# Optimization experiments

Measured on AMD Instinct MI355X. Metric: run time of the kernel, lower is better.

Reference implementation:

```python
import jax, jax.numpy as jnp
import numpy as np

N = 50000          # nodes
E = 800000         # edges (before self loops)
C_IN, HID, C_OUT, L = 128, 64, 64, 3
LSTM_H = (L * HID) // 2   # 96, PyG JK-LSTM hidden size
NEG_SLOPE = 0.2


def gat_conv(x, src, dst, W, a_src, a_dst, b):
    # single-head PyG GATConv
    h = x @ W.T                                  # [N, HID]
    al = h @ a_src                               # [N] src attention logits
    ar = h @ a_dst                               # [N]
    e = jax.nn.leaky_relu(al[src] + ar[dst], NEG_SLOPE)   # [E+N]
    m = jax.ops.segment_max(e, dst, num_segments=N)
    ex = jnp.exp(e - m[dst])
    den = jax.ops.segment_sum(ex, dst, num_segments=N)
    coef = ex / den[dst]                         # segment softmax over dst neighborhoods
    out = jax.ops.segment_sum(coef[:, None] * h[src], dst, num_segments=N)
    return out + b


def lstm_dir(seq, Wih, Whh, bih, bhh, reverse):
    # seq: [L, N, C]; returns hidden states [L, N, H] in original time order
    H = Whh.shape[1]
    h0 = jnp.zeros((seq.shape[1], H), seq.dtype)

    def step(carry, x_t):
        h, c = carry
        g = x_t @ Wih.T + bih + h @ Whh.T + bhh
        i, f, gg, o = jnp.split(g, 4, axis=-1)
        c = jax.nn.sigmoid(f) * c + jax.nn.sigmoid(i) * jnp.tanh(gg)
        h = jax.nn.sigmoid(o) * jnp.tanh(c)
        return (h, c), h

    _, hs = jax.lax.scan(step, (h0, h0), seq, reverse=reverse)
    return hs


def setup_inputs() -> dict:
    key = jax.random.key(0)
    ks = jax.random.split(key, 32)
    s = 0.1
    inp = {
        'x': jax.random.normal(ks[0], (N, C_IN), jnp.float32),
        'edge_index': jax.random.randint(ks[1], (2, E), 0, N, jnp.int64
                                         if jax.config.jax_enable_x64 else jnp.int32),
    }
    dims = [C_IN, HID, HID]
    for l in range(L):
        inp[f'conv{l}_W'] = s * jax.random.normal(ks[2 + 4 * l], (HID, dims[l]), jnp.float32)
        inp[f'conv{l}_asrc'] = s * jax.random.normal(ks[3 + 4 * l], (HID,), jnp.float32)
        inp[f'conv{l}_adst'] = s * jax.random.normal(ks[4 + 4 * l], (HID,), jnp.float32)
        inp[f'conv{l}_b'] = jnp.zeros((HID,), jnp.float32)
    for d, off in (('f', 16), ('b', 20)):
        inp[f'lstm_Wih_{d}'] = s * jax.random.normal(ks[off], (4 * LSTM_H, HID), jnp.float32)
        inp[f'lstm_Whh_{d}'] = s * jax.random.normal(ks[off + 1], (4 * LSTM_H, LSTM_H), jnp.float32)
        inp[f'lstm_bih_{d}'] = jnp.zeros((4 * LSTM_H,), jnp.float32)
        inp[f'lstm_bhh_{d}'] = jnp.zeros((4 * LSTM_H,), jnp.float32)
    inp['att_W'] = s * jax.random.normal(ks[24], (1, 2 * LSTM_H), jnp.float32)
    inp['att_b'] = jnp.zeros((1,), jnp.float32)
    inp['out_W'] = s * jax.random.normal(ks[25], (C_OUT, HID), jnp.float32)
    inp['out_b'] = jnp.zeros((C_OUT,), jnp.float32)
    return inp


def reference(x, edge_index,
              conv0_W, conv0_asrc, conv0_adst, conv0_b,
              conv1_W, conv1_asrc, conv1_adst, conv1_b,
              conv2_W, conv2_asrc, conv2_adst, conv2_b,
              lstm_Wih_f, lstm_Whh_f, lstm_bih_f, lstm_bhh_f,
              lstm_Wih_b, lstm_Whh_b, lstm_bih_b, lstm_bhh_b,
              att_W, att_b, out_W, out_b):
    # add self loops (PyG GATConv default)
    loop = jnp.arange(N, dtype=edge_index.dtype)
    src = jnp.concatenate([edge_index[0], loop])
    dst = jnp.concatenate([edge_index[1], loop])

    convs = [(conv0_W, conv0_asrc, conv0_adst, conv0_b),
             (conv1_W, conv1_asrc, conv1_adst, conv1_b),
             (conv2_W, conv2_asrc, conv2_adst, conv2_b)]
    xs = []
    h = x
    for (W, asrc, adst, b) in convs:
        h = jax.nn.relu(gat_conv(h, src, dst, W, asrc, adst, b))
        xs.append(h)

    seq = jnp.stack(xs, axis=0)                       # [L, N, HID]
    hf = lstm_dir(seq, lstm_Wih_f, lstm_Whh_f, lstm_bih_f, lstm_bhh_f, False)
    hb = lstm_dir(seq, lstm_Wih_b, lstm_Whh_b, lstm_bih_b, lstm_bhh_b, True)
    hcat = jnp.concatenate([hf, hb], axis=-1)         # [L, N, 2*LSTM_H]
    logits = (hcat @ att_W.T + att_b)[..., 0]         # [L, N]
    alpha = jax.nn.softmax(logits, axis=0)            # softmax over layers
    agg = jnp.einsum('lnc,ln->nc', seq, alpha)        # [N, HID]
    return agg @ out_W.T + out_b
```

## Files before the change

### kernel.cpp

```cpp
#include <hip/hip_runtime.h>
#include <hip/hip_bf16.h>
#include <math.h>


typedef __attribute__((ext_vector_type(4))) float f32x4;
typedef __attribute__((ext_vector_type(8))) short bf16x8;

__device__ __forceinline__ float rcp_f(float x) {
    return __builtin_amdgcn_rcpf(x);
}
__device__ __forceinline__ float sigmoid_f(float x) {
    return rcp_f(1.0f + __expf(-x));
}
__device__ __forceinline__ float tanh_f(float x) {
    return fmaf(2.0f, rcp_f(1.0f + __expf(-2.0f * x)), -1.0f);
}
__device__ __forceinline__ unsigned short f2bf(float x) {
    union { float f; unsigned int u; } v; v.f = x;
    unsigned int r = (v.u + 0x7FFFu + ((v.u >> 16) & 1u)) >> 16;
    return (unsigned short)r;
}
__device__ __forceinline__ float bf2f(unsigned short u) {
    union { unsigned int i; float f; } v; v.i = ((unsigned int)u) << 16;
    return v.f;
}

template<int K>
__global__ __launch_bounds__(256) void lin_kernel(
    const float* __restrict__ x, const float* __restrict__ W,
    const float* __restrict__ asrc, const float* __restrict__ adst,
    unsigned short* __restrict__ h, float* __restrict__ al,
    float* __restrict__ ar, int N)
{
    __shared__ __align__(16) float Wl[64][K + 4];
    for (int i = threadIdx.x; i < 64 * K; i += 256)
        Wl[i / K][i % K] = W[i];
    __syncthreads();

    int lane = threadIdx.x & 63;
    float as = asrc[lane], ad = adst[lane];
    int wid = (blockIdx.x * 256 + threadIdx.x) >> 6;
    int nw  = (gridDim.x * 256) >> 6;
    int n4max = (N + 3) >> 2;
    for (int n4 = wid; n4 < n4max; n4 += nw) {
        int nb = __builtin_amdgcn_readfirstlane(n4) << 2;
        const float* xr0 = x + (size_t)nb * K;
        const float* xr1 = x + (size_t)min(nb + 1, N - 1) * K;
        const float* xr2 = x + (size_t)min(nb + 2, N - 1) * K;
        const float* xr3 = x + (size_t)min(nb + 3, N - 1) * K;
        float a0 = 0.f, a1 = 0.f, a2 = 0.f, a3 = 0.f;
        #pragma unroll 4
        for (int k = 0; k < K; k += 4) {
            f32x4 wv = *reinterpret_cast<const f32x4*>(&Wl[lane][k]);
            float4 x0 = *reinterpret_cast<const float4*>(xr0 + k);
            float4 x1 = *reinterpret_cast<const float4*>(xr1 + k);
            float4 x2 = *reinterpret_cast<const float4*>(xr2 + k);
            float4 x3 = *reinterpret_cast<const float4*>(xr3 + k);
            a0 += x0.x * wv.x + x0.y * wv.y + x0.z * wv.z + x0.w * wv.w;
            a1 += x1.x * wv.x + x1.y * wv.y + x1.z * wv.z + x1.w * wv.w;
            a2 += x2.x * wv.x + x2.y * wv.y + x2.z * wv.z + x2.w * wv.w;
            a3 += x3.x * wv.x + x3.y * wv.y + x3.z * wv.z + x3.w * wv.w;
        }
        float accs[4] = {a0, a1, a2, a3};
        #pragma unroll
        for (int j = 0; j < 4; ++j) {
            int n = nb + j;
            if (n >= N) break;
            float acc = accs[j];
            h[(size_t)n * 64 + lane] = f2bf(acc);
            float pa = acc * as, pr = acc * ad;
            #pragma unroll
            for (int off = 32; off > 0; off >>= 1) {
                pa += __shfl_down(pa, off);
                pr += __shfl_down(pr, off);
            }
            if (lane == 0) { al[n] = pa; ar[n] = pr; }
        }
    }
}

__global__ void csr_zero(int* __restrict__ deg, int* __restrict__ cursor, int N)
{
    int i = blockIdx.x * blockDim.x + threadIdx.x;
    if (i < N) { deg[i] = 0; cursor[i] = 0; }
}

__global__ void csr_hist(const int* __restrict__ dst, int* __restrict__ deg, int E)
{
    int i = blockIdx.x * blockDim.x + threadIdx.x;
    if (i < E) atomicAdd(&deg[dst[i]], 1);
}

__global__ void csr_scan1(const int* __restrict__ deg, int* __restrict__ incl,
                          int* __restrict__ part, int N)
{
    __shared__ int sb[2][256];
    int tid = threadIdx.x;
    int i = blockIdx.x * 256 + tid;
    int v = (i < N) ? deg[i] + 1 : 0;
    sb[0][tid] = v;
    __syncthreads();
    int cur = 0;
    #pragma unroll
    for (int off = 1; off < 256; off <<= 1) {
        int s = sb[cur][tid];
        if (tid >= off) s += sb[cur][tid - off];
        sb[cur ^ 1][tid] = s;
        cur ^= 1;
        __syncthreads();
    }
    if (i < N) incl[i] = sb[cur][tid];
    if (tid == 255) part[blockIdx.x] = sb[cur][255];
}

__global__ void csr_scan2(int* __restrict__ part, int NB)
{
    __shared__ int sb[2][256];
    int tid = threadIdx.x;
    int v = (tid < NB) ? part[tid] : 0;
    sb[0][tid] = v;
    __syncthreads();
    int cur = 0;
    #pragma unroll
    for (int off = 1; off < 256; off <<= 1) {
        int s = sb[cur][tid];
        if (tid >= off) s += sb[cur][tid - off];
        sb[cur ^ 1][tid] = s;
        cur ^= 1;
        __syncthreads();
    }
    if (tid < NB) part[tid] = sb[cur][tid] - v;
}

__global__ void csr_scan3(const int* __restrict__ deg, const int* __restrict__ incl,
                          const int* __restrict__ part, int* __restrict__ rowptr,
                          int N, int total)
{
    int i = blockIdx.x * blockDim.x + threadIdx.x;
    if (i < N)
        rowptr[i] = part[i >> 8] + incl[i] - (deg[i] + 1);
    if (i == 0) rowptr[N] = total;
}

__global__ void csr_scatter(const int* __restrict__ src, const int* __restrict__ dst,
                            const int* __restrict__ rowptr, int* __restrict__ cursor,
                            int* __restrict__ csr_src, int E, int N)
{
    int i = blockIdx.x * blockDim.x + threadIdx.x;
    if (i >= E + N) return;
    int s = (i < E) ? src[i] : (i - E);
    int d = (i < E) ? dst[i] : (i - E);
    int pos = atomicAdd(&cursor[d], 1);
    csr_src[rowptr[d] + pos] = s;
}

__global__ __launch_bounds__(256) void agg_kernel(
    const int* __restrict__ rowptr, const int* __restrict__ csr_src,
    const float* __restrict__ al, const float* __restrict__ ar,
    const unsigned short* __restrict__ h, const float* __restrict__ b,
    float* __restrict__ outseq, unsigned short* __restrict__ outseq_bf, int N)
{
    int lane = threadIdx.x & 63;
    int w = threadIdx.x >> 6;
    int li = lane & 15, grp = lane >> 4;
    int d = blockIdx.x * 16 + w * 4 + grp;
    if (d >= N) return;

    int rp0 = rowptr[d], rp1 = rowptr[d + 1];
    int degd = rp1 - rp0;
    float ard = ar[d];
    float den = 0.0f;
    float a0 = 0.f, a1 = 0.f, a2 = 0.f, a3 = 0.f;
    const int grpbase = grp << 4;

    for (int c0 = 0; c0 < degd; c0 += 16) {
        int ne = min(16, degd - c0);
        int s_l = 0;
        float ex_l = 0.0f;
        if (li < ne) {
            s_l = csr_src[rp0 + c0 + li];
            float e = al[s_l] + ard;
            e = (e >= 0.0f) ? e : 0.2f * e;
            ex_l = __expf(e);
        }
        float dsum = ex_l;
        dsum += __shfl_xor(dsum, 1);
        dsum += __shfl_xor(dsum, 2);
        dsum += __shfl_xor(dsum, 4);
        dsum += __shfl_xor(dsum, 8);
        den += dsum;
        #pragma unroll 4
        for (int e2 = 0; e2 < ne; ++e2) {
            int sl = grpbase + e2;
            float exb = __shfl(ex_l, sl);
            int sb = __shfl(s_l, sl);
            uint2 hv = *reinterpret_cast<const uint2*>(
                &h[(size_t)sb * 64 + li * 4]);
            a0 += exb * bf2f((unsigned short)(hv.x & 0xFFFFu));
            a1 += exb * bf2f((unsigned short)(hv.x >> 16));
            a2 += exb * bf2f((unsigned short)(hv.y & 0xFFFFu));
            a3 += exb * bf2f((unsigned short)(hv.y >> 16));
        }
    }
    float inv = rcp_f(den);
    int ch = li * 4;
    float4 v;
    v.x = fmaxf(fmaf(a0, inv, b[ch]),     0.0f);
    v.y = fmaxf(fmaf(a1, inv, b[ch + 1]), 0.0f);
    v.z = fmaxf(fmaf(a2, inv, b[ch + 2]), 0.0f);
    v.w = fmaxf(fmaf(a3, inv, b[ch + 3]), 0.0f);
    *reinterpret_cast<float4*>(&outseq[(size_t)d * 64 + ch]) = v;
    uint2 bb;
    bb.x = (unsigned int)f2bf(v.x) | ((unsigned int)f2bf(v.y) << 16);
    bb.y = (unsigned int)f2bf(v.z) | ((unsigned int)f2bf(v.w) << 16);
    *reinterpret_cast<uint2*>(&outseq_bf[(size_t)d * 64 + ch]) = bb;
}

__global__ void prep_lstm(
    const float* __restrict__ WihF, const float* __restrict__ WhhF,
    const float* __restrict__ bihF, const float* __restrict__ bhhF,
    const float* __restrict__ WihB_, const float* __restrict__ WhhB_,
    const float* __restrict__ bihB_, const float* __restrict__ bhhB_,
    unsigned short* __restrict__ WB, float* __restrict__ bsum)
{
    int tid = blockIdx.x * blockDim.x + threadIdx.x;
    if (tid < 2 * 61440) {
        int dir = tid / 61440, rr = tid % 61440;
        const float* Wih = dir ? WihB_ : WihF;
        const float* Whh = dir ? WhhB_ : WhhF;
        float v;
        if (rr < 24576) {
            int f = rr >> 9, l = (rr >> 3) & 63, s = rr & 7;
            int kc = f & 1, qt = f >> 1;
            int q = qt / 6, t6 = qt % 6;
            int j = q * 96 + t6 * 16 + (l & 15);
            int k = kc * 32 + (l >> 4) * 8 + s;
            v = Wih[j * 64 + k];
        } else {
            int rr2 = rr - 24576;
            int f = rr2 >> 9, l = (rr2 >> 3) & 63, s = rr2 & 7;
            int kc = f % 3, qt = f / 3;
            int q = qt / 6, t6 = qt % 6;
            int j = q * 96 + t6 * 16 + (l & 15);
            int k = kc * 32 + (l >> 4) * 8 + s;
            v = Whh[j * 96 + k];
        }
        WB[tid] = f2bf(v);
    } else if (tid < 2 * 61440 + 2 * 384) {
        int q2 = tid - 2 * 61440;
        int dir = q2 / 384, j = q2 % 384;
        bsum[q2] = dir ? (bihB_[j] + bhhB_[j]) : (bihF[j] + bhhF[j]);
    }
}

__global__ __launch_bounds__(512, 2) void lstm_kernel(
    const unsigned short* __restrict__ seq_bf,
    const unsigned short* __restrict__ WB,
    const float* __restrict__ bsum, const float* __restrict__ attW,
    const float* __restrict__ attb, const float* __restrict__ outW,
    const float* __restrict__ outb, float* __restrict__ out, int N)
{
    __shared__ __align__(16) unsigned short smem[75520];
    unsigned short* WL = smem;
    unsigned short* HS = smem + 61440;
    float* LG = reinterpret_cast<float*>(smem + 74752);

    const int tid  = threadIdx.x;
    const int lane = tid & 63;
    const int w    = tid >> 6;
    const int i16  = lane & 15;
    const int g    = lane >> 4;
    const int n0   = blockIdx.x * 128;
    const int nodebase = 16 * w;
    const int myrow = nodebase + g * 4;

    float attb0 = attb[0];
    if (tid < 384) LG[tid] = attb0;

    for (int dir = 0; dir < 2; ++dir) {
        __syncthreads();
        {
            const f32x4* gsrc = reinterpret_cast<const f32x4*>(WB + dir * 61440);
            f32x4* ldst = reinterpret_cast<f32x4*>(WL);
            #pragma unroll
            for (int it = 0; it < 15; ++it)
                ldst[it * 512 + tid] = gsrc[it * 512 + tid];
        }
        {
            unsigned int* hz = reinterpret_cast<unsigned int*>(&HS[nodebase * 104]);
            for (int e2 = lane; e2 < 832; e2 += 64) hz[e2] = 0u;
        }
        const float* bs = bsum + dir * 384;
        const float* aw = attW + dir * 96;
        float bsr[24];
        #pragma unroll
        for (int t6 = 0; t6 < 6; ++t6)
            #pragma unroll
            for (int q = 0; q < 4; ++q)
                bsr[t6 * 4 + q] = bs[q * 96 + t6 * 16 + i16];
        float awr[6];
        #pragma unroll
        for (int t6 = 0; t6 < 6; ++t6) awr[t6] = aw[t6 * 16 + i16];
        float c[24];
        #pragma unroll
        for (int a = 0; a < 24; ++a) c[a] = 0.0f;
        __syncthreads();

        for (int step = 0; step < 3; ++step) {
            int t = dir ? (2 - step) : step;

            int nn = n0 + nodebase + i16;
            nn = (nn < N) ? nn : (N - 1);
            const unsigned short* xr = seq_bf + ((size_t)t * N + nn) * 64 + g * 8;
            bf16x8 ax0 = *reinterpret_cast<const bf16x8*>(xr);
            bf16x8 ax1 = *reinterpret_cast<const bf16x8*>(xr + 32);

            const unsigned short* hrow = &HS[(nodebase + i16) * 104];
            bf16x8 ah0 = *reinterpret_cast<const bf16x8*>(hrow + g * 8);
            bf16x8 ah1 = *reinterpret_cast<const bf16x8*>(hrow + 32 + g * 8);
            bf16x8 ah2 = *reinterpret_cast<const bf16x8*>(hrow + 64 + g * 8);
            const unsigned short* wbase = WL + lane * 8;

            float lp[4] = {0.0f, 0.0f, 0.0f, 0.0f};
            #pragma unroll
            for (int t6 = 0; t6 < 6; ++t6) {
                const int jb = t6 * 16 + i16;
                f32x4 acc4[4];
                #pragma unroll
                for (int q = 0; q < 4; ++q) {
                    float bv = bsr[t6 * 4 + q];
                    acc4[q] = (f32x4){bv, bv, bv, bv};
                }
                #pragma unroll
                for (int q = 0; q < 4; ++q) {
                    const int qt = q * 6 + t6;
                    const unsigned short* wih = wbase + (qt * 2) * 512;
                    const unsigned short* whh = wbase + 24576 + (qt * 3) * 512;
                    acc4[q] = __builtin_amdgcn_mfma_f32_16x16x32_bf16(
                        ax0, *reinterpret_cast<const bf16x8*>(wih), acc4[q], 0, 0, 0);
                    acc4[q] = __builtin_amdgcn_mfma_f32_16x16x32_bf16(
                        ax1, *reinterpret_cast<const bf16x8*>(wih + 512), acc4[q], 0, 0, 0);
                    acc4[q] = __builtin_amdgcn_mfma_f32_16x16x32_bf16(
                        ah0, *reinterpret_cast<const bf16x8*>(whh), acc4[q], 0, 0, 0);
                    acc4[q] = __builtin_amdgcn_mfma_f32_16x16x32_bf16(
                        ah1, *reinterpret_cast<const bf16x8*>(whh + 512), acc4[q], 0, 0, 0);
                    acc4[q] = __builtin_amdgcn_mfma_f32_16x16x32_bf16(
                        ah2, *reinterpret_cast<const bf16x8*>(whh + 1024), acc4[q], 0, 0, 0);
                }
                #pragma unroll
                for (int reg = 0; reg < 4; ++reg) {
                    float ii = acc4[0][reg];
                    float ff = acc4[1][reg];
                    float gg = acc4[2][reg];
                    float oo = acc4[3][reg];
                    float cn = sigmoid_f(ff) * c[t6 * 4 + reg]
                             + sigmoid_f(ii) * tanh_f(gg);
                    c[t6 * 4 + reg] = cn;
                    float hn = sigmoid_f(oo) * tanh_f(cn);
                    HS[(myrow + reg) * 104 + jb] = f2bf(hn);
                    lp[reg] += hn * awr[t6];
                }
            }
            #pragma unroll
            for (int reg = 0; reg < 4; ++reg) {
                float v = lp[reg];
                v += __shfl_xor(v, 1);
                v += __shfl_xor(v, 2);
                v += __shfl_xor(v, 4);
                v += __shfl_xor(v, 8);
                if (i16 == 0) LG[t * 128 + myrow + reg] += v;
            }
        }
    }
    __syncthreads();

    float* alphaF = reinterpret_cast<float*>(HS);
    if (tid < 128) {
        float l0 = LG[tid], l1 = LG[128 + tid], l2 = LG[256 + tid];
        float mx = fmaxf(fmaxf(l0, l1), l2);
        float e0 = __expf(l0 - mx), e1 = __expf(l1 - mx), e2 = __expf(l2 - mx);
        float inv = rcp_f(e0 + e1 + e2);
        alphaF[tid] = e0 * inv; alphaF[128 + tid] = e1 * inv;
        alphaF[256 + tid] = e2 * inv;
    }
    __syncthreads();

    float* aggF = reinterpret_cast<float*>(WL);
    for (int idx = tid; idx < 128 * 64; idx += 512) {
        int r = idx >> 6, k = idx & 63;
        int n = n0 + r;
        float v = 0.0f;
        if (n < N) {
            float a0 = alphaF[r], a1 = alphaF[128 + r], a2 = alphaF[256 + r];
            v = a0 * bf2f(seq_bf[((size_t)n) * 64 + k])
              + a1 * bf2f(seq_bf[((size_t)N + n) * 64 + k])
              + a2 * bf2f(seq_bf[((size_t)2 * N + n) * 64 + k]);
        }
        aggF[r * 68 + k] = v;
    }
    __syncthreads();

    f32x4 ow[16];
    #pragma unroll
    for (int kk = 0; kk < 16; ++kk)
        ow[kk] = *reinterpret_cast<const f32x4*>(&outW[(size_t)lane * 64 + kk * 4]);
    float ob = outb[lane];
    for (int r = w; r < 128; r += 8) {
        int n = n0 + r;
        if (n >= N) break;
        float a = ob;
        #pragma unroll
        for (int kk = 0; kk < 16; ++kk) {
            f32x4 av = *reinterpret_cast<const f32x4*>(&aggF[r * 68 + kk * 4]);
            a += ow[kk].x * av.x + ow[kk].y * av.y
               + ow[kk].z * av.z + ow[kk].w * av.w;
        }
        out[(size_t)n * 64 + lane] = a;
    }
}

extern "C" void kernel_launch(void* const* d_in, const int* in_sizes, int n_in,
                              void* d_out, int out_size, void* d_ws, size_t ws_size,
                              hipStream_t stream)
{
    const float* x    = (const float*)d_in[0];
    const int*   ei   = (const int*)d_in[1];
    const float* convW[3]  = {(const float*)d_in[2], (const float*)d_in[6],  (const float*)d_in[10]};
    const float* convAs[3] = {(const float*)d_in[3], (const float*)d_in[7],  (const float*)d_in[11]};
    const float* convAd[3] = {(const float*)d_in[4], (const float*)d_in[8],  (const float*)d_in[12]};
    const float* convB[3]  = {(const float*)d_in[5], (const float*)d_in[9],  (const float*)d_in[13]};
    const float* WihF = (const float*)d_in[14];
    const float* WhhF = (const float*)d_in[15];
    const float* bihF = (const float*)d_in[16];
    const float* bhhF = (const float*)d_in[17];
    const float* WihB = (const float*)d_in[18];
    const float* WhhB = (const float*)d_in[19];
    const float* bihB = (const float*)d_in[20];
    const float* bhhB = (const float*)d_in[21];
    const float* attW = (const float*)d_in[22];
    const float* attb = (const float*)d_in[23];
    const float* outW = (const float*)d_in[24];
    const float* outb = (const float*)d_in[25];

    int N = in_sizes[0] / 128;
    int E = in_sizes[1] / 2;
    const int* src = ei;
    const int* dst = ei + E;
    int total = E + N;

    float* w = (float*)d_ws;
    float* seq  = w;  w += (size_t)3 * N * 64;
    unsigned short* h_bf = (unsigned short*)w;  w += (size_t)N * 32;
    float* al   = w;  w += N;
    float* ar   = w;  w += N;
    float* bsum = w;  w += 768;
    unsigned short* WB = (unsigned short*)w;  w += 61440;
    unsigned short* seq_bf = (unsigned short*)w;  w += (size_t)3 * N * 32;
    int* deg     = (int*)w;        w += N;
    int* cursor  = (int*)w;        w += N;
    int* rowptr  = (int*)w;        w += (N + 1);
    int* incl    = (int*)w;        w += N;
    int* part    = (int*)w;        w += 256;
    int* csr_src = (int*)w;        w += total;

    int NB = (N + 255) / 256;

    csr_zero<<<NB, 256, 0, stream>>>(deg, cursor, N);
    csr_hist<<<(E + 255) / 256, 256, 0, stream>>>(dst, deg, E);
    csr_scan1<<<NB, 256, 0, stream>>>(deg, incl, part, N);
    csr_scan2<<<1, 256, 0, stream>>>(part, NB);
    csr_scan3<<<NB, 256, 0, stream>>>(deg, incl, part, rowptr, N, total);
    csr_scatter<<<(total + 255) / 256, 256, 0, stream>>>(src, dst, rowptr, cursor,
                                                         csr_src, E, N);

    prep_lstm<<<(2 * 61440 + 768 + 255) / 256, 256, 0, stream>>>(
        WihF, WhhF, bihF, bhhF, WihB, WhhB, bihB, bhhB, WB, bsum);

    for (int l = 0; l < 3; ++l) {
        const float* in = (l == 0) ? x : seq + (size_t)(l - 1) * N * 64;
        if (l == 0)
            lin_kernel<128><<<2048, 256, 0, stream>>>(in, convW[l], convAs[l], convAd[l],
                                                      h_bf, al, ar, N);
        else
            lin_kernel<64><<<2048, 256, 0, stream>>>(in, convW[l], convAs[l], convAd[l],
                                                     h_bf, al, ar, N);
        agg_kernel<<<(N + 15) / 16, 256, 0, stream>>>(rowptr, csr_src, al, ar, h_bf,
                                                      convB[l], seq + (size_t)l * N * 64,
                                                      seq_bf + (size_t)l * N * 64, N);
    }

    lstm_kernel<<<(N + 127) / 128, 512, 0, stream>>>(seq_bf, WB, bsum, attW, attb,
                                                     outW, outb, (float*)d_out, N);
}
```

Before: 374.1 us.

## Process two 128-node tiles per LSTM block to amortize weight staging

Each LSTM block now handles two consecutive 128-node tiles, and the grid size is halved. The per-direction bf16 weight load into shared memory is therefore shared across both tiles instead of being repeated for every tile. The logits buffer is doubled so each tile keeps its own LSTM attention scores. The cost is fewer blocks (about 196 on a 256-CU part), which can leave CUs idle and lower parallelism, and the serialized epilogue adds extra barriers.

```diff
diff --git a/kernel.cpp b/kernel.cpp
--- a/kernel.cpp
+++ b/kernel.cpp
@@ -260,7 +260,7 @@
     const float* __restrict__ attb, const float* __restrict__ outW,
     const float* __restrict__ outb, float* __restrict__ out, int N)
 {
-    __shared__ __align__(16) unsigned short smem[75520];
+    __shared__ __align__(16) unsigned short smem[76288];
     unsigned short* WL = smem;
     unsigned short* HS = smem + 61440;
     float* LG = reinterpret_cast<float*>(smem + 74752);
@@ -270,12 +270,12 @@
     const int w    = tid >> 6;
     const int i16  = lane & 15;
     const int g    = lane >> 4;
-    const int n0   = blockIdx.x * 128;
     const int nodebase = 16 * w;
     const int myrow = nodebase + g * 4;
+    const int U = (N + 127) >> 7;
 
     float attb0 = attb[0];
-    if (tid < 384) LG[tid] = attb0;
+    for (int idx = tid; idx < 768; idx += 512) LG[idx] = attb0;
 
     for (int dir = 0; dir < 2; ++dir) {
         __syncthreads();
@@ -285,10 +285,6 @@
             #pragma unroll
             for (int it = 0; it < 15; ++it)
                 ldst[it * 512 + tid] = gsrc[it * 512 + tid];
-        }
-        {
-            unsigned int* hz = reinterpret_cast<unsigned int*>(&HS[nodebase * 104]);
-            for (int e2 = lane; e2 < 832; e2 += 64) hz[e2] = 0u;
         }
         const float* bs = bsum + dir * 384;
         const float* aw = attW + dir * 96;
@@ -301,102 +297,90 @@
         float awr[6];
         #pragma unroll
         for (int t6 = 0; t6 < 6; ++t6) awr[t6] = aw[t6 * 16 + i16];
-        float c[24];
+        __syncthreads();
+
         #pragma unroll
-        for (int a = 0; a < 24; ++a) c[a] = 0.0f;
-        __syncthreads();
-
-        for (int step = 0; step < 3; ++step) {
-            int t = dir ? (2 - step) : step;
-
-            int nn = n0 + nodebase + i16;
-            nn = (nn < N) ? nn : (N - 1);
-            const unsigned short* xr = seq_bf + ((size_t)t * N + nn) * 64 + g * 8;
-            bf16x8 ax0 = *reinterpret_cast<const bf16x8*>(xr);
-            bf16x8 ax1 = *reinterpret_cast<const bf16x8*>(xr + 32);
-
-            const unsigned short* hrow = &HS[(nodebase + i16) * 104];
-            bf16x8 ah0 = *reinterpret_cast<const bf16x8*>(hrow + g * 8);
-            bf16x8 ah1 = *reinterpret_cast<const bf16x8*>(hrow + 32 + g * 8);
-            bf16x8 ah2 = *reinterpret_cast<const bf16x8*>(hrow + 64 + g * 8);
-            const unsigned short* wbase = WL + lane * 8;
-
-            float lp[4] = {0.0f, 0.0f, 0.0f, 0.0f};
+        for (int un = 0; un < 2; ++un) {
+            int u = blockIdx.x * 2 + un;
+            if (u >= U) continue;
+            int n0 = u * 128;
+
+            {
+                unsigned int* hz =
+                    reinterpret_cast<unsigned int*>(&HS[nodebase * 104]);
+                for (int e2 = lane; e2 < 832; e2 += 64) hz[e2] = 0u;
+            }
+            float c[24];
             #pragma unroll
-            for (int t6 = 0; t6 < 6; ++t6) {
-                const int jb = t6 * 16 + i16;
-                f32x4 acc4[4];
+            for (int a = 0; a < 24; ++a) c[a] = 0.0f;
+
+            for (int step = 0; step < 3; ++step) {
+                int t = dir ? (2 - step) : step;
+
+                int nn = n0 + nodebase + i16;
+                nn = (nn < N) ? nn : (N - 1);
+                const unsigned short* xr =
+                    seq_bf + ((size_t)t * N + nn) * 64 + g * 8;
+                bf16x8 ax0 = *reinterpret_cast<const bf16x8*>(xr);
+                bf16x8 ax1 = *reinterpret_cast<const bf16x8*>(xr + 32);
+
+                const unsigned short* hrow = &HS[(nodebase + i16) * 104];
+                bf16x8 ah0 = *reinterpret_cast<const bf16x8*>(hrow + g * 8);
+                bf16x8 ah1 = *reinterpret_cast<const bf16x8*>(hrow + 32 + g * 8);
+                bf16x8 ah2 = *reinterpret_cast<const bf16x8*>(hrow + 64 + g * 8);
+                const unsigned short* wbase = WL + lane * 8;
+
+                float lp[4] = {0.0f, 0.0f, 0.0f, 0.0f};
                 #pragma unroll
-                for (int q = 0; q < 4; ++q) {
-                    float bv = bsr[t6 * 4 + q];
-                    acc4[q] = (f32x4){bv, bv, bv, bv};
-                }
-                #pragma unroll
-                for (int q = 0; q < 4; ++q) {
-                    const int qt = q * 6 + t6;
-                    const unsigned short* wih = wbase + (qt * 2) * 512;
-                    const unsigned short* whh = wbase + 24576 + (qt * 3) * 512;
-                    acc4[q] = __builtin_amdgcn_mfma_f32_16x16x32_bf16(
-                        ax0, *reinterpret_cast<const bf16x8*>(wih), acc4[q], 0, 0, 0);
-                    acc4[q] = __builtin_amdgcn_mfma_f32_16x16x32_bf16(
-                        ax1, *reinterpret_cast<const bf16x8*>(wih + 512), acc4[q], 0, 0, 0);
-                    acc4[q] = __builtin_amdgcn_mfma_f32_16x16x32_bf16(
-                        ah0, *reinterpret_cast<const bf16x8*>(whh), acc4[q], 0, 0, 0);
-                    acc4[q] = __builtin_amdgcn_mfma_f32_16x16x32_bf16(
-                        ah1, *reinterpret_cast<const bf16x8*>(whh + 512), acc4[q], 0, 0, 0);
-                    acc4[q] = __builtin_amdgcn_mfma_f32_16x16x32_bf16(
-                        ah2, *reinterpret_cast<const bf16x8*>(whh + 1024), acc4[q], 0, 0, 0);
+                for (int t6 = 0; t6 < 6; ++t6) {
+                    const int jb = t6 * 16 + i16;
+                    f32x4 acc4[4];
+                    #pragma unroll
+                    for (int q = 0; q < 4; ++q) {
+                        float bv = bsr[t6 * 4 + q];
+                        acc4[q] = (f32x4){bv, bv, bv, bv};
+                    }
+                    #pragma unroll
+                    for (int q = 0; q < 4; ++q) {
+                        const int qt = q * 6 + t6;
+                        const unsigned short* wih = wbase + (qt * 2) * 512;
+                        const unsigned short* whh = wbase + 24576 + (qt * 3) * 512;
+                        acc4[q] = __builtin_amdgcn_mfma_f32_16x16x32_bf16(
+                            ax0, *reinterpret_cast<const bf16x8*>(wih), acc4[q], 0, 0, 0);
+                        acc4[q] = __builtin_amdgcn_mfma_f32_16x16x32_bf16(
+                            ax1, *reinterpret_cast<const bf16x8*>(wih + 512), acc4[q], 0, 0, 0);
+                        acc4[q] = __builtin_amdgcn_mfma_f32_16x16x32_bf16(
+                            ah0, *reinterpret_cast<const bf16x8*>(whh), acc4[q], 0, 0, 0);
+                        acc4[q] = __builtin_amdgcn_mfma_f32_16x16x32_bf16(
+                            ah1, *reinterpret_cast<const bf16x8*>(whh + 512), acc4[q], 0, 0, 0);
+                        acc4[q] = __builtin_amdgcn_mfma_f32_16x16x32_bf16(
+                            ah2, *reinterpret_cast<const bf16x8*>(whh + 1024), acc4[q], 0, 0, 0);
+                    }
+                    #pragma unroll
+                    for (int reg = 0; reg < 4; ++reg) {
+                        float ii = acc4[0][reg];
+                        float ff = acc4[1][reg];
+                        float gg = acc4[2][reg];
+                        float oo = acc4[3][reg];
+                        float cn = sigmoid_f(ff) * c[t6 * 4 + reg]
+                                 + sigmoid_f(ii) * tanh_f(gg);
+                        c[t6 * 4 + reg] = cn;
+                        float hn = sigmoid_f(oo) * tanh_f(cn);
+                        HS[(myrow + reg) * 104 + jb] = f2bf(hn);
+                        lp[reg] += hn * awr[t6];
+                    }
                 }
                 #pragma unroll
                 for (int reg = 0; reg < 4; ++reg) {
-                    float ii = acc4[0][reg];
-                    float ff = acc4[1][reg];
-                    float gg = acc4[2][reg];
-                    float oo = acc4[3][reg];
-                    float cn = sigmoid_f(ff) * c[t6 * 4 + reg]
-                             + sigmoid_f(ii) * tanh_f(gg);
-                    c[t6 * 4 + reg] = cn;
-                    float hn = sigmoid_f(oo) * tanh_f(cn);
-                    HS[(myrow + reg) * 104 + jb] = f2bf(hn);
-                    lp[reg] += hn * awr[t6];
+                    float v = lp[reg];
+                    v += __shfl_xor(v, 1);
+                    v += __shfl_xor(v, 2);
+                    v += __shfl_xor(v, 4);
+                    v += __shfl_xor(v, 8);
+                    if (i16 == 0) LG[un * 384 + t * 128 + myrow + reg] += v;
                 }
             }
-            #pragma unroll
-            for (int reg = 0; reg < 4; ++reg) {
-                float v = lp[reg];
-                v += __shfl_xor(v, 1);
-                v += __shfl_xor(v, 2);
-                v += __shfl_xor(v, 4);
-                v += __shfl_xor(v, 8);
-                if (i16 == 0) LG[t * 128 + myrow + reg] += v;
-            }
-        }
-    }
-    __syncthreads();
-
-    float* alphaF = reinterpret_cast<float*>(HS);
-    if (tid < 128) {
-        float l0 = LG[tid], l1 = LG[128 + tid], l2 = LG[256 + tid];
-        float mx = fmaxf(fmaxf(l0, l1), l2);
-        float e0 = __expf(l0 - mx), e1 = __expf(l1 - mx), e2 = __expf(l2 - mx);
-        float inv = rcp_f(e0 + e1 + e2);
-        alphaF[tid] = e0 * inv; alphaF[128 + tid] = e1 * inv;
-        alphaF[256 + tid] = e2 * inv;
-    }
-    __syncthreads();
-
-    float* aggF = reinterpret_cast<float*>(WL);
-    for (int idx = tid; idx < 128 * 64; idx += 512) {
-        int r = idx >> 6, k = idx & 63;
-        int n = n0 + r;
-        float v = 0.0f;
-        if (n < N) {
-            float a0 = alphaF[r], a1 = alphaF[128 + r], a2 = alphaF[256 + r];
-            v = a0 * bf2f(seq_bf[((size_t)n) * 64 + k])
-              + a1 * bf2f(seq_bf[((size_t)N + n) * 64 + k])
-              + a2 * bf2f(seq_bf[((size_t)2 * N + n) * 64 + k]);
-        }
-        aggF[r * 68 + k] = v;
+        }
     }
     __syncthreads();
 
@@ -405,17 +389,53 @@
     for (int kk = 0; kk < 16; ++kk)
         ow[kk] = *reinterpret_cast<const f32x4*>(&outW[(size_t)lane * 64 + kk * 4]);
     float ob = outb[lane];
-    for (int r = w; r < 128; r += 8) {
-        int n = n0 + r;
-        if (n >= N) break;
-        float a = ob;
-        #pragma unroll
-        for (int kk = 0; kk < 16; ++kk) {
-            f32x4 av = *reinterpret_cast<const f32x4*>(&aggF[r * 68 + kk * 4]);
-            a += ow[kk].x * av.x + ow[kk].y * av.y
-               + ow[kk].z * av.z + ow[kk].w * av.w;
-        }
-        out[(size_t)n * 64 + lane] = a;
+
+    for (int un = 0; un < 2; ++un) {
+        int u = blockIdx.x * 2 + un;
+        if (u >= U) continue;
+        int n0 = u * 128;
+
+        float* alphaF = reinterpret_cast<float*>(HS);
+        if (tid < 128) {
+            float l0 = LG[un * 384 + tid];
+            float l1 = LG[un * 384 + 128 + tid];
+            float l2 = LG[un * 384 + 256 + tid];
+            float mx = fmaxf(fmaxf(l0, l1), l2);
+            float e0 = __expf(l0 - mx), e1 = __expf(l1 - mx), e2 = __expf(l2 - mx);
+            float inv = rcp_f(e0 + e1 + e2);
+            alphaF[tid] = e0 * inv; alphaF[128 + tid] = e1 * inv;
+            alphaF[256 + tid] = e2 * inv;
+        }
+        __syncthreads();
+
+        float* aggF = reinterpret_cast<float*>(WL);
+        for (int idx = tid; idx < 128 * 64; idx += 512) {
+            int r = idx >> 6, k = idx & 63;
+            int n = n0 + r;
+            float v = 0.0f;
+            if (n < N) {
+                float a0 = alphaF[r], a1 = alphaF[128 + r], a2 = alphaF[256 + r];
+                v = a0 * bf2f(seq_bf[((size_t)n) * 64 + k])
+                  + a1 * bf2f(seq_bf[((size_t)N + n) * 64 + k])
+                  + a2 * bf2f(seq_bf[((size_t)2 * N + n) * 64 + k]);
+            }
+            aggF[r * 68 + k] = v;
+        }
+        __syncthreads();
+
+        for (int r = w; r < 128; r += 8) {
+            int n = n0 + r;
+            if (n >= N) break;
+            float a = ob;
+            #pragma unroll
+            for (int kk = 0; kk < 16; ++kk) {
+                f32x4 av = *reinterpret_cast<const f32x4*>(&aggF[r * 68 + kk * 4]);
+                a += ow[kk].x * av.x + ow[kk].y * av.y
+                   + ow[kk].z * av.z + ow[kk].w * av.w;
+            }
+            out[(size_t)n * 64 + lane] = a;
+        }
+        __syncthreads();
     }
 }
 
@@ -489,6 +509,7 @@
                                                       seq_bf + (size_t)l * N * 64, N);
     }
 
-    lstm_kernel<<<(N + 127) / 128, 512, 0, stream>>>(seq_bf, WB, bsum, attW, attb,
-                                                     outW, outb, (float*)d_out, N);
-}
+    int U = (N + 127) / 128;
+    lstm_kernel<<<(U + 1) / 2, 512, 0, stream>>>(seq_bf, WB, bsum, attW, attb,
+                                                 outW, outb, (float*)d_out, N);
+}
```

New measurement: 375.4 us. About the same (+0.3%).

## Split GAT aggregation lanes across edges and channel quarters

Applied to the files above, without the earlier changes.

Reorganizes the per-destination aggregation so each 16-lane group processes 4 edges at once, with each lane loading 16 bf16 channels (32 bytes) of a source row instead of 4 channels per edge serially. Partial sums are combined with xor shuffles at the end, and one lane per channel quarter writes the outputs. This is meant to cut the serial per-edge loop and the per-edge broadcast shuffles and to widen memory loads. In exchange it needs 16 accumulator registers per lane, a final reduction, and wastes lanes on the tail when the degree is not a multiple of 4.

```diff
diff --git a/kernel.cpp b/kernel.cpp
--- a/kernel.cpp
+++ b/kernel.cpp
@@ -165,55 +165,72 @@
     int li = lane & 15, grp = lane >> 4;
     int d = blockIdx.x * 16 + w * 4 + grp;
     if (d >= N) return;
+    int cq = li >> 2, es = li & 3;
 
     int rp0 = rowptr[d], rp1 = rowptr[d + 1];
     int degd = rp1 - rp0;
     float ard = ar[d];
     float den = 0.0f;
-    float a0 = 0.f, a1 = 0.f, a2 = 0.f, a3 = 0.f;
-    const int grpbase = grp << 4;
-
-    for (int c0 = 0; c0 < degd; c0 += 16) {
-        int ne = min(16, degd - c0);
-        int s_l = 0;
-        float ex_l = 0.0f;
-        if (li < ne) {
-            s_l = csr_src[rp0 + c0 + li];
-            float e = al[s_l] + ard;
-            e = (e >= 0.0f) ? e : 0.2f * e;
-            ex_l = __expf(e);
-        }
-        float dsum = ex_l;
-        dsum += __shfl_xor(dsum, 1);
-        dsum += __shfl_xor(dsum, 2);
-        dsum += __shfl_xor(dsum, 4);
-        dsum += __shfl_xor(dsum, 8);
-        den += dsum;
-        #pragma unroll 4
-        for (int e2 = 0; e2 < ne; ++e2) {
-            int sl = grpbase + e2;
-            float exb = __shfl(ex_l, sl);
-            int sb = __shfl(s_l, sl);
-            uint2 hv = *reinterpret_cast<const uint2*>(
-                &h[(size_t)sb * 64 + li * 4]);
-            a0 += exb * bf2f((unsigned short)(hv.x & 0xFFFFu));
-            a1 += exb * bf2f((unsigned short)(hv.x >> 16));
-            a2 += exb * bf2f((unsigned short)(hv.y & 0xFFFFu));
-            a3 += exb * bf2f((unsigned short)(hv.y >> 16));
-        }
-    }
-    float inv = rcp_f(den);
-    int ch = li * 4;
-    float4 v;
-    v.x = fmaxf(fmaf(a0, inv, b[ch]),     0.0f);
-    v.y = fmaxf(fmaf(a1, inv, b[ch + 1]), 0.0f);
-    v.z = fmaxf(fmaf(a2, inv, b[ch + 2]), 0.0f);
-    v.w = fmaxf(fmaf(a3, inv, b[ch + 3]), 0.0f);
-    *reinterpret_cast<float4*>(&outseq[(size_t)d * 64 + ch]) = v;
-    uint2 bb;
-    bb.x = (unsigned int)f2bf(v.x) | ((unsigned int)f2bf(v.y) << 16);
-    bb.y = (unsigned int)f2bf(v.z) | ((unsigned int)f2bf(v.w) << 16);
-    *reinterpret_cast<uint2*>(&outseq_bf[(size_t)d * 64 + ch]) = bb;
+    float acc16[16];
+    #pragma unroll
+    for (int j = 0; j < 16; ++j) acc16[j] = 0.0f;
+
+    for (int c0 = 0; c0 < degd; c0 += 4) {
+        int e = c0 + es;
+        int s = csr_src[rp0 + min(e, degd - 1)];
+        float exv = 0.0f;
+        if (e < degd) {
+            float t = al[s] + ard;
+            t = (t >= 0.0f) ? t : 0.2f * t;
+            exv = __expf(t);
+        }
+        den += exv;
+        const uint4* hp = reinterpret_cast<const uint4*>(
+            &h[(size_t)s * 64 + cq * 16]);
+        uint4 h0 = hp[0];
+        uint4 h1 = hp[1];
+        #pragma unroll
+        for (int j = 0; j < 4; ++j) {
+            unsigned int v0 = (&h0.x)[j];
+            acc16[j * 2]     += exv * bf2f((unsigned short)(v0 & 0xFFFFu));
+            acc16[j * 2 + 1] += exv * bf2f((unsigned short)(v0 >> 16));
+            unsigned int v1 = (&h1.x)[j];
+            acc16[8 + j * 2]     += exv * bf2f((unsigned short)(v1 & 0xFFFFu));
+            acc16[8 + j * 2 + 1] += exv * bf2f((unsigned short)(v1 >> 16));
+        }
+    }
+    den += __shfl_xor(den, 1);
+    den += __shfl_xor(den, 2);
+    #pragma unroll
+    for (int j = 0; j < 16; ++j) {
+        acc16[j] += __shfl_xor(acc16[j], 1);
+        acc16[j] += __shfl_xor(acc16[j], 2);
+    }
+    if (es == 0) {
+        float inv = rcp_f(den);
+        int ch = cq * 16;
+        float vo[16];
+        #pragma unroll
+        for (int j = 0; j < 16; ++j)
+            vo[j] = fmaxf(fmaf(acc16[j], inv, b[ch + j]), 0.0f);
+        #pragma unroll
+        for (int j4 = 0; j4 < 4; ++j4) {
+            float4 fv = make_float4(vo[j4 * 4], vo[j4 * 4 + 1],
+                                    vo[j4 * 4 + 2], vo[j4 * 4 + 3]);
+            *reinterpret_cast<float4*>(&outseq[(size_t)d * 64 + ch + j4 * 4]) = fv;
+        }
+        uint4 b0, b1;
+        b0.x = (unsigned int)f2bf(vo[0])  | ((unsigned int)f2bf(vo[1])  << 16);
+        b0.y = (unsigned int)f2bf(vo[2])  | ((unsigned int)f2bf(vo[3])  << 16);
+        b0.z = (unsigned int)f2bf(vo[4])  | ((unsigned int)f2bf(vo[5])  << 16);
+        b0.w = (unsigned int)f2bf(vo[6])  | ((unsigned int)f2bf(vo[7])  << 16);
+        b1.x = (unsigned int)f2bf(vo[8])  | ((unsigned int)f2bf(vo[9])  << 16);
+        b1.y = (unsigned int)f2bf(vo[10]) | ((unsigned int)f2bf(vo[11]) << 16);
+        b1.z = (unsigned int)f2bf(vo[12]) | ((unsigned int)f2bf(vo[13]) << 16);
+        b1.w = (unsigned int)f2bf(vo[14]) | ((unsigned int)f2bf(vo[15]) << 16);
+        *reinterpret_cast<uint4*>(&outseq_bf[(size_t)d * 64 + ch]) = b0;
+        *reinterpret_cast<uint4*>(&outseq_bf[(size_t)d * 64 + ch + 8]) = b1;
+    }
 }
 
 __global__ void prep_lstm(
```

Result: no change. 377.6 us (+0.9%).
